# Performance work log

Hardware: AMD Instinct MI355X
Metric: run time of the kernel (lower is better)

Reference implementation:

```python
import jax, jax.numpy as jnp
import numpy as np

N = 50000          # total atoms in batch
E = 1_600_000      # total edges (flattened neighbor list)
ELEM = 64          # elem_fea_len
NBR = 32           # nbr_fea_len
EPS = 1e-5         # BatchNorm eps


def _batchnorm(x, gamma, beta):
    # training-mode BatchNorm1d: per-feature batch stats (biased variance)
    mean = x.mean(axis=0)
    var = ((x - mean) ** 2).mean(axis=0)
    return gamma * (x - mean) * jax.lax.rsqrt(var + EPS) + beta


def setup_inputs() -> dict:
    key = jax.random.key(0)
    ks = jax.random.split(key, 6)
    atom_in_fea = jax.random.normal(ks[0], (N, ELEM), jnp.float32)
    nbr_fea = jax.random.normal(ks[1], (E, NBR), jnp.float32)
    self_fea_idx = jnp.sort(jax.random.randint(ks[2], (E,), 0, N))
    nbr_fea_idx = jax.random.randint(ks[3], (E,), 0, N)
    fan_in = 2 * ELEM + NBR
    W = jax.random.normal(ks[4], (fan_in, 2 * ELEM), jnp.float32) * (1.0 / np.sqrt(fan_in))
    b = jnp.zeros((2 * ELEM,), jnp.float32)
    gamma1 = jnp.ones((2 * ELEM,), jnp.float32)
    beta1 = jnp.zeros((2 * ELEM,), jnp.float32)
    gamma2 = jnp.ones((ELEM,), jnp.float32)
    beta2 = jnp.zeros((ELEM,), jnp.float32)
    return {
        "atom_in_fea": atom_in_fea,
        "nbr_fea": nbr_fea,
        "self_fea_idx": self_fea_idx,
        "nbr_fea_idx": nbr_fea_idx,
        "W": W,
        "b": b,
        "gamma1": gamma1,
        "beta1": beta1,
        "gamma2": gamma2,
        "beta2": beta2,
    }


def reference(atom_in_fea, nbr_fea, self_fea_idx, nbr_fea_idx,
              W, b, gamma1, beta1, gamma2, beta2):
    # gather + concat: (E, 2*ELEM + NBR)
    total_fea = jnp.concatenate(
        [atom_in_fea[self_fea_idx], atom_in_fea[nbr_fea_idx], nbr_fea], axis=1)
    total_fea = total_fea @ W + b                    # fc_full: (E, 2*ELEM)
    total_fea = _batchnorm(total_fea, gamma1, beta1)  # bn1
    filter_fea, core_fea = jnp.split(total_fea, 2, axis=1)
    nbr_msg = jax.nn.sigmoid(filter_fea) * jax.nn.softplus(core_fea)  # (E, ELEM)
    nbr_sumed = jax.ops.segment_sum(nbr_msg, self_fea_idx, num_segments=N)
    nbr_sumed = _batchnorm(nbr_sumed, gamma2, beta2)  # bn2
    return jax.nn.softplus(atom_in_fea + nbr_sumed)   # residual + softplus2
```

## Files before the change

### kernel.cpp

```cpp
#include <hip/hip_runtime.h>

#define E_TOT 1600000
#define N_AT  50000
#define NB1   (E_TOT / 128)

typedef unsigned short u16;
typedef __attribute__((ext_vector_type(8))) __bf16 bf16x8;
typedef __attribute__((ext_vector_type(4))) __bf16 bf16x4;
typedef __attribute__((ext_vector_type(4))) float f32x4;

#define SUM1_OFF 0
#define SUM2_OFF 1024
#define WF_OFF   2048
#define NS_OFF   43008
#define AB_OFF   12843008
#define NBRB_OFF 19243008
#define PART_OFF 121643008

__device__ __forceinline__ u16 f2bf(float f) {
    unsigned int u = __float_as_uint(f);
    return (u16)((u + 0x7FFFu + ((u >> 16) & 1u)) >> 16);
}
__device__ __forceinline__ float softplus_f(float x) {
    return fmaxf(x, 0.0f) + __logf(1.0f + __expf(-fabsf(x)));
}
__device__ __forceinline__ bf16x8 cvt8v(f32x4 a, f32x4 b) {
    bf16x8 r;
    r[0] = (__bf16)a[0]; r[1] = (__bf16)a[1]; r[2] = (__bf16)a[2]; r[3] = (__bf16)a[3];
    r[4] = (__bf16)b[0]; r[5] = (__bf16)b[1]; r[6] = (__bf16)b[2]; r[7] = (__bf16)b[3];
    return r;
}
__device__ __forceinline__ void ldsdma16(void* lds, const void* g) {
    __builtin_amdgcn_global_load_lds(
        (const __attribute__((address_space(1))) unsigned int*)g,
        (__attribute__((address_space(3))) unsigned int*)lds, 16, 0, 0);
}

__global__ __launch_bounds__(256) void k_setup(const float* __restrict__ atom,
                                               const float* __restrict__ W,
                                               char* __restrict__ ws) {
    u16* wf   = (u16*)(ws + WF_OFF);
    float* ns = (float*)(ws + NS_OFF);
    u16* ab   = (u16*)(ws + AB_OFF);
    const int tid = blockIdx.x * 256 + threadIdx.x;
    const int gsz = gridDim.x * 256;

    for (int i = tid; i < 512; i += gsz) ((float*)ws)[i] = 0.0f;

    f32x4 z = {0.f, 0.f, 0.f, 0.f};
    for (int i = tid; i < N_AT * 64 / 4; i += gsz) ((f32x4*)ns)[i] = z;

    for (int i = tid; i < N_AT * 64 / 4; i += gsz) {
        f32x4 v = ((const f32x4*)atom)[i];
        bf16x4 h;
        h[0] = (__bf16)v[0]; h[1] = (__bf16)v[1];
        h[2] = (__bf16)v[2]; h[3] = (__bf16)v[3];
        *(bf16x4*)(ab + i * 4) = h;
    }

    for (int t = tid; t < 20480; t += gsz) {
        int j = t & 7, l2 = (t >> 3) & 63, ct = (t >> 9) & 7, kt = t >> 12;
        int k = kt * 32 + (l2 >> 4) * 8 + j;
        int c = ct * 16 + (l2 & 15);
        wf[t] = f2bf(W[k * 128 + c]);
    }
}

__global__ __launch_bounds__(512, 6) void k1_stats(const u16* __restrict__ ab,
                                                   const float* __restrict__ nbr,
                                                   u16* __restrict__ nbrb,
                                                   const int* __restrict__ sidx,
                                                   const int* __restrict__ nidx,
                                                   const u16* __restrict__ wf,
                                                   float* __restrict__ part) {
    __shared__ __align__(16) u16 bsm[20480];
    __shared__ float bs[256];
    const int tx = threadIdx.x, lane = tx & 63, w = tx >> 6;
    const int mrow = lane & 15, quad = lane >> 4;

#pragma unroll
    for (int i = 0; i < 5; i++) {
        int off = (i * 512 + tx) * 16;
        ldsdma16((char*)bsm + off, (const char*)wf + off);
    }

    const int r0 = blockIdx.x * 128 + w * 16 + mrow;
    const int s0 = sidx[r0];
    const int n0 = nidx[r0];
    const u16* pa0 = ab + (size_t)s0 * 64 + quad * 8;
    const u16* pb0 = ab + (size_t)n0 * 64 + quad * 8;
    const float* p0 = nbr + (size_t)r0 * 32 + quad * 8;

    bf16x8 a0 = *(const bf16x8*)(pa0);
    bf16x8 a1 = *(const bf16x8*)(pa0 + 32);
    bf16x8 a2 = *(const bf16x8*)(pb0);
    bf16x8 a3 = *(const bf16x8*)(pb0 + 32);
    bf16x8 a4 = cvt8v(*(const f32x4*)p0, *(const f32x4*)(p0 + 4));
    *(bf16x8*)(nbrb + (size_t)r0 * 32 + quad * 8) = a4;

    if (tx < 256) bs[tx] = 0.0f;
    __syncthreads();

    f32x4 acc[8];
#pragma unroll
    for (int ct = 0; ct < 8; ct++) { f32x4 z = {0.f, 0.f, 0.f, 0.f}; acc[ct] = z; }

#pragma unroll
    for (int kt = 0; kt < 5; kt++) {
        bf16x8 a = (kt == 0) ? a0 : (kt == 1) ? a1 : (kt == 2) ? a2 : (kt == 3) ? a3 : a4;
#pragma unroll
        for (int ct = 0; ct < 8; ct++) {
            bf16x8 b = *(const bf16x8*)&bsm[((kt * 8 + ct) * 64 + lane) * 8];
            acc[ct] = __builtin_amdgcn_mfma_f32_16x16x32_bf16(a, b, acc[ct], 0, 0, 0);
        }
    }

#pragma unroll
    for (int ct = 0; ct < 8; ct++) {
        float s = 0.f, q = 0.f;
#pragma unroll
        for (int rg = 0; rg < 4; rg++) {
            float v = acc[ct][rg];
            s += v; q += v * v;
        }
        s += __shfl_xor(s, 16, 64); s += __shfl_xor(s, 32, 64);
        q += __shfl_xor(q, 16, 64); q += __shfl_xor(q, 32, 64);
        if (quad == 0) {
            atomicAdd(&bs[ct * 16 + mrow], s);
            atomicAdd(&bs[128 + ct * 16 + mrow], q);
        }
    }
    __syncthreads();
    if (tx < 256) part[(size_t)blockIdx.x * 256 + tx] = bs[tx];
}

__global__ __launch_bounds__(256) void k2_red(const float* __restrict__ part,
                                              float* __restrict__ sums1) {
    const int tx = threadIdx.x;
    float s = 0.f;
    for (int r = blockIdx.x; r < NB1; r += 256) s += part[(size_t)r * 256 + tx];
    atomicAdd(&sums1[tx], s);
}

__global__ __launch_bounds__(512, 6) void k3_msg(const u16* __restrict__ ab,
                                                 const u16* __restrict__ nbrb,
                                                 const int* __restrict__ sidx,
                                                 const int* __restrict__ nidx,
                                                 const u16* __restrict__ wf,
                                                 const float* __restrict__ sums1,
                                                 const float* __restrict__ g1,
                                                 const float* __restrict__ b1,
                                                 float* __restrict__ ns) {
    __shared__ __align__(16) char smraw[40960];
    u16* bsm = (u16*)smraw;
    float (*msgb)[16 * 66] = (float(*)[16 * 66])smraw;
    const int tx = threadIdx.x, lane = tx & 63, w = tx >> 6;
    const int mrow = lane & 15, quad = lane >> 4;

#pragma unroll
    for (int i = 0; i < 5; i++) {
        int off = (i * 512 + tx) * 16;
        ldsdma16(smraw + off, (const char*)wf + off);
    }

    const int rb = blockIdx.x * 128 + w * 16;
    const int r0 = rb + mrow;
    const int s0 = sidx[r0];
    const int n0 = nidx[r0];
    const u16* pa0 = ab + (size_t)s0 * 64 + quad * 8;
    const u16* pb0 = ab + (size_t)n0 * 64 + quad * 8;

    bf16x8 a0 = *(const bf16x8*)(pa0);
    bf16x8 a1 = *(const bf16x8*)(pa0 + 32);
    bf16x8 a2 = *(const bf16x8*)(pb0);
    bf16x8 a3 = *(const bf16x8*)(pb0 + 32);
    bf16x8 a4 = *(const bf16x8*)(nbrb + (size_t)r0 * 32 + quad * 8);

    __syncthreads();

    f32x4 acc[8];
#pragma unroll
    for (int ct = 0; ct < 8; ct++) { f32x4 z = {0.f, 0.f, 0.f, 0.f}; acc[ct] = z; }

#pragma unroll
    for (int kt = 0; kt < 5; kt++) {
        bf16x8 a = (kt == 0) ? a0 : (kt == 1) ? a1 : (kt == 2) ? a2 : (kt == 3) ? a3 : a4;
#pragma unroll
        for (int ct = 0; ct < 8; ct++) {
            bf16x8 b = *(const bf16x8*)&bsm[((kt * 8 + ct) * 64 + lane) * 8];
            acc[ct] = __builtin_amdgcn_mfma_f32_16x16x32_bf16(a, b, acc[ct], 0, 0, 0);
        }
    }

    const float invE = 1.0f / (float)E_TOT;
    float af[4], kf[4], ac[4], kc[4];
#pragma unroll
    for (int ct = 0; ct < 4; ct++) {
        int cf = ct * 16 + mrow, cc = cf + 64;
        float mf = sums1[cf] * invE;
        float vf = sums1[128 + cf] * invE - mf * mf;
        af[ct] = g1[cf] * rsqrtf(vf + 1e-5f);
        kf[ct] = b1[cf] - af[ct] * mf;
        float mc = sums1[cc] * invE;
        float vc = sums1[128 + cc] * invE - mc * mc;
        ac[ct] = g1[cc] * rsqrtf(vc + 1e-5f);
        kc[ct] = b1[cc] - ac[ct] * mc;
    }

    __syncthreads();

    float* mw = msgb[w];
#pragma unroll
    for (int ct = 0; ct < 4; ct++) {
#pragma unroll
        for (int rg = 0; rg < 4; rg++) {
            float xf = af[ct] * acc[ct][rg] + kf[ct];
            float xc = ac[ct] * acc[ct + 4][rg] + kc[ct];
            float sg = 1.0f / (1.0f + __expf(-xf));
            mw[(quad * 4 + rg) * 66 + ct * 16 + mrow] = sg * softplus_f(xc);
        }
    }

    float accum = 0.f;
    int cur = sidx[rb];
#pragma unroll
    for (int i = 0; i < 16; i++) {
        int idx = sidx[rb + i];
        if (idx != cur) {
            atomicAdd(&ns[(size_t)cur * 64 + lane], accum);
            accum = 0.f;
            cur = idx;
        }
        accum += mw[i * 66 + lane];
    }
    atomicAdd(&ns[(size_t)cur * 64 + lane], accum);
}

__global__ __launch_bounds__(256) void k4_bn2stats(const float* __restrict__ ns,
                                                   float* __restrict__ sums2) {
    const int tx = threadIdx.x;
    const int col = tx & 63, rg = tx >> 6;
    float s = 0.f, q = 0.f;
    for (int r = blockIdx.x * 4 + rg; r < N_AT; r += 256 * 4) {
        float v = ns[r * 64 + col];
        s += v; q += v * v;
    }
    atomicAdd(&sums2[col], s);
    atomicAdd(&sums2[64 + col], q);
}

__global__ __launch_bounds__(256) void k5_final(const float* __restrict__ atom,
                                                const float* __restrict__ ns,
                                                const float* __restrict__ sums2,
                                                const float* __restrict__ g2,
                                                const float* __restrict__ b2,
                                                float* __restrict__ out) {
    const int i = blockIdx.x * 256 + threadIdx.x;
    const int col = i & 63;
    const float invN = 1.0f / (float)N_AT;
    float mean = sums2[col] * invN;
    float var = sums2[64 + col] * invN - mean * mean;
    float a2 = g2[col] * rsqrtf(var + 1e-5f);
    float c2 = b2[col] - a2 * mean;
    out[i] = softplus_f(atom[i] + a2 * ns[i] + c2);
}

extern "C" void kernel_launch(void* const* d_in, const int* in_sizes, int n_in,
                              void* d_out, int out_size, void* d_ws, size_t ws_size,
                              hipStream_t stream) {
    const float* atom = (const float*)d_in[0];
    const float* nbr  = (const float*)d_in[1];
    const int* sidx   = (const int*)d_in[2];
    const int* nidx   = (const int*)d_in[3];
    const float* W    = (const float*)d_in[4];
    const float* g1   = (const float*)d_in[6];
    const float* b1   = (const float*)d_in[7];
    const float* g2   = (const float*)d_in[8];
    const float* b2   = (const float*)d_in[9];
    float* out = (float*)d_out;

    char* ws = (char*)d_ws;
    float* sums1 = (float*)(ws + SUM1_OFF);
    float* sums2 = (float*)(ws + SUM2_OFF);
    u16*   wf    = (u16*)(ws + WF_OFF);
    float* nsum  = (float*)(ws + NS_OFF);
    u16*   ab    = (u16*)(ws + AB_OFF);
    u16*   nbrb  = (u16*)(ws + NBRB_OFF);
    float* part  = (float*)(ws + PART_OFF);

    k_setup<<<1024, 256, 0, stream>>>(atom, W, ws);
    k1_stats<<<NB1, 512, 0, stream>>>(ab, nbr, nbrb, sidx, nidx, wf, part);
    k2_red<<<256, 256, 0, stream>>>(part, sums1);
    k3_msg<<<NB1, 512, 0, stream>>>(ab, nbrb, sidx, nidx, wf, sums1, g1, b1, nsum);
    k4_bn2stats<<<256, 256, 0, stream>>>(nsum, sums2);
    k5_final<<<(N_AT * 64) / 256, 256, 0, stream>>>(atom, nsum, sums2, g2, b2, out);
}
```

Baseline: 709.2 us.

## Precompute per-atom projections of W and gather them per edge

```diff
diff --git a/kernel.cpp b/kernel.cpp
--- a/kernel.cpp
+++ b/kernel.cpp
@@ -6,20 +6,23 @@
 
 typedef unsigned short u16;
 typedef __attribute__((ext_vector_type(8))) __bf16 bf16x8;
-typedef __attribute__((ext_vector_type(4))) __bf16 bf16x4;
 typedef __attribute__((ext_vector_type(4))) float f32x4;
 
 #define SUM1_OFF 0
 #define SUM2_OFF 1024
-#define WF_OFF   2048
+#define WF3_OFF  2048
+#define WF12_OFF 10240
 #define NS_OFF   43008
-#define AB_OFF   12843008
-#define NBRB_OFF 19243008
-#define PART_OFF 121643008
+#define P12_OFF  12843008
+#define NBRB_OFF 38443008
+#define PART_OFF 140843008
 
 __device__ __forceinline__ u16 f2bf(float f) {
     unsigned int u = __float_as_uint(f);
     return (u16)((u + 0x7FFFu + ((u >> 16) & 1u)) >> 16);
+}
+__device__ __forceinline__ float bfu(u16 v) {
+    return __uint_as_float(((unsigned int)v) << 16);
 }
 __device__ __forceinline__ float softplus_f(float x) {
     return fmaxf(x, 0.0f) + __logf(1.0f + __expf(-fabsf(x)));
@@ -36,12 +39,11 @@
         (__attribute__((address_space(3))) unsigned int*)lds, 16, 0, 0);
 }
 
-__global__ __launch_bounds__(256) void k_setup(const float* __restrict__ atom,
-                                               const float* __restrict__ W,
+__global__ __launch_bounds__(256) void k_setup(const float* __restrict__ W,
                                                char* __restrict__ ws) {
-    u16* wf   = (u16*)(ws + WF_OFF);
+    u16* wf3  = (u16*)(ws + WF3_OFF);
+    u16* wf12 = (u16*)(ws + WF12_OFF);
     float* ns = (float*)(ws + NS_OFF);
-    u16* ab   = (u16*)(ws + AB_OFF);
     const int tid = blockIdx.x * 256 + threadIdx.x;
     const int gsz = gridDim.x * 256;
 
@@ -50,69 +52,113 @@
     f32x4 z = {0.f, 0.f, 0.f, 0.f};
     for (int i = tid; i < N_AT * 64 / 4; i += gsz) ((f32x4*)ns)[i] = z;
 
-    for (int i = tid; i < N_AT * 64 / 4; i += gsz) {
-        f32x4 v = ((const f32x4*)atom)[i];
-        bf16x4 h;
-        h[0] = (__bf16)v[0]; h[1] = (__bf16)v[1];
-        h[2] = (__bf16)v[2]; h[3] = (__bf16)v[3];
-        *(bf16x4*)(ab + i * 4) = h;
-    }
-
-    for (int t = tid; t < 20480; t += gsz) {
-        int j = t & 7, l2 = (t >> 3) & 63, ct = (t >> 9) & 7, kt = t >> 12;
+    for (int t = tid; t < 4096; t += gsz) {
+        int j = t & 7, l2 = (t >> 3) & 63, ct = (t >> 9) & 7;
+        int k = 128 + (l2 >> 4) * 8 + j;
+        int c = ct * 16 + (l2 & 15);
+        wf3[t] = f2bf(W[k * 128 + c]);
+    }
+    for (int t = tid; t < 16384; t += gsz) {
+        int j = t & 7, l2 = (t >> 3) & 63, ct = (t >> 9) & 15, kt = t >> 13;
         int k = kt * 32 + (l2 >> 4) * 8 + j;
         int c = ct * 16 + (l2 & 15);
-        wf[t] = f2bf(W[k * 128 + c]);
-    }
-}
-
-__global__ __launch_bounds__(512, 6) void k1_stats(const u16* __restrict__ ab,
-                                                   const float* __restrict__ nbr,
+        wf12[t] = f2bf(c < 128 ? W[k * 128 + c] : W[(64 + k) * 128 + (c - 128)]);
+    }
+}
+
+__global__ __launch_bounds__(512, 4) void k_p12(const float* __restrict__ atom,
+                                                const u16* __restrict__ wf12,
+                                                u16* __restrict__ p12) {
+    __shared__ __align__(16) u16 bsm[16384];
+    const int tx = threadIdx.x, lane = tx & 63, w = tx >> 6;
+    const int mrow = lane & 15, quad = lane >> 4;
+
+#pragma unroll
+    for (int i = 0; i < 4; i++) {
+        int off = (i * 512 + tx) * 16;
+        ldsdma16((char*)bsm + off, (const char*)wf12 + off);
+    }
+
+    const int rb = blockIdx.x * 128 + w * 16;
+    const int r0 = rb + mrow;
+    const int rr = r0 < N_AT ? r0 : N_AT - 1;
+    const float* pa = atom + (size_t)rr * 64 + quad * 8;
+
+    __syncthreads();
+
+    bf16x8 a0 = cvt8v(*(const f32x4*)pa, *(const f32x4*)(pa + 4));
+    bf16x8 a1 = cvt8v(*(const f32x4*)(pa + 32), *(const f32x4*)(pa + 36));
+
+    f32x4 acc[16];
+#pragma unroll
+    for (int ct = 0; ct < 16; ct++) { f32x4 zz = {0.f, 0.f, 0.f, 0.f}; acc[ct] = zz; }
+
+#pragma unroll
+    for (int kt = 0; kt < 2; kt++) {
+        bf16x8 a = kt ? a1 : a0;
+#pragma unroll
+        for (int ct = 0; ct < 16; ct++) {
+            bf16x8 b = *(const bf16x8*)&bsm[((kt * 16 + ct) * 64 + lane) * 8];
+            acc[ct] = __builtin_amdgcn_mfma_f32_16x16x32_bf16(a, b, acc[ct], 0, 0, 0);
+        }
+    }
+
+#pragma unroll
+    for (int ct = 0; ct < 16; ct++) {
+#pragma unroll
+        for (int rg = 0; rg < 4; rg++) {
+            int r = rb + quad * 4 + rg;
+            if (r < N_AT) p12[(size_t)r * 256 + ct * 16 + mrow] = f2bf(acc[ct][rg]);
+        }
+    }
+}
+
+__global__ __launch_bounds__(512, 6) void k1_stats(const float* __restrict__ nbr,
                                                    u16* __restrict__ nbrb,
                                                    const int* __restrict__ sidx,
                                                    const int* __restrict__ nidx,
-                                                   const u16* __restrict__ wf,
+                                                   const u16* __restrict__ wf3,
+                                                   const u16* __restrict__ p12,
                                                    float* __restrict__ part) {
-    __shared__ __align__(16) u16 bsm[20480];
+    __shared__ __align__(16) u16 bsm[4096];
     __shared__ float bs[256];
     const int tx = threadIdx.x, lane = tx & 63, w = tx >> 6;
     const int mrow = lane & 15, quad = lane >> 4;
 
-#pragma unroll
-    for (int i = 0; i < 5; i++) {
-        int off = (i * 512 + tx) * 16;
-        ldsdma16((char*)bsm + off, (const char*)wf + off);
-    }
-
-    const int r0 = blockIdx.x * 128 + w * 16 + mrow;
-    const int s0 = sidx[r0];
-    const int n0 = nidx[r0];
-    const u16* pa0 = ab + (size_t)s0 * 64 + quad * 8;
-    const u16* pb0 = ab + (size_t)n0 * 64 + quad * 8;
+    { int off = tx * 16; ldsdma16((char*)bsm + off, (const char*)wf3 + off); }
+
+    const int rb = blockIdx.x * 128 + w * 16;
+    const int r0 = rb + mrow;
+    const int e0 = rb + quad * 4;
+    int s_[4], n_[4];
+#pragma unroll
+    for (int rg = 0; rg < 4; rg++) { s_[rg] = sidx[e0 + rg]; n_[rg] = nidx[e0 + rg]; }
     const float* p0 = nbr + (size_t)r0 * 32 + quad * 8;
-
-    bf16x8 a0 = *(const bf16x8*)(pa0);
-    bf16x8 a1 = *(const bf16x8*)(pa0 + 32);
-    bf16x8 a2 = *(const bf16x8*)(pb0);
-    bf16x8 a3 = *(const bf16x8*)(pb0 + 32);
-    bf16x8 a4 = cvt8v(*(const f32x4*)p0, *(const f32x4*)(p0 + 4));
-    *(bf16x8*)(nbrb + (size_t)r0 * 32 + quad * 8) = a4;
 
     if (tx < 256) bs[tx] = 0.0f;
     __syncthreads();
 
+    f32x4 nlo = *(const f32x4*)p0;
+    f32x4 nhi = *(const f32x4*)(p0 + 4);
+    bf16x8 a4 = cvt8v(nlo, nhi);
+    *(bf16x8*)(nbrb + (size_t)r0 * 32 + quad * 8) = a4;
+
     f32x4 acc[8];
 #pragma unroll
-    for (int ct = 0; ct < 8; ct++) { f32x4 z = {0.f, 0.f, 0.f, 0.f}; acc[ct] = z; }
-
-#pragma unroll
-    for (int kt = 0; kt < 5; kt++) {
-        bf16x8 a = (kt == 0) ? a0 : (kt == 1) ? a1 : (kt == 2) ? a2 : (kt == 3) ? a3 : a4;
-#pragma unroll
-        for (int ct = 0; ct < 8; ct++) {
-            bf16x8 b = *(const bf16x8*)&bsm[((kt * 8 + ct) * 64 + lane) * 8];
-            acc[ct] = __builtin_amdgcn_mfma_f32_16x16x32_bf16(a, b, acc[ct], 0, 0, 0);
-        }
+    for (int ct = 0; ct < 8; ct++) { f32x4 zz = {0.f, 0.f, 0.f, 0.f}; acc[ct] = zz; }
+#pragma unroll
+    for (int ct = 0; ct < 8; ct++) {
+        bf16x8 b = *(const bf16x8*)&bsm[(ct * 64 + lane) * 8];
+        acc[ct] = __builtin_amdgcn_mfma_f32_16x16x32_bf16(a4, b, acc[ct], 0, 0, 0);
+    }
+
+#pragma unroll
+    for (int rg = 0; rg < 4; rg++) {
+        const u16* q1 = p12 + (size_t)s_[rg] * 256 + mrow;
+        const u16* q2 = p12 + (size_t)n_[rg] * 256 + 128 + mrow;
+#pragma unroll
+        for (int ct = 0; ct < 8; ct++)
+            acc[ct][rg] += bfu(q1[ct * 16]) + bfu(q2[ct * 16]);
     }
 
 #pragma unroll
@@ -142,54 +188,49 @@
     atomicAdd(&sums1[tx], s);
 }
 
-__global__ __launch_bounds__(512, 6) void k3_msg(const u16* __restrict__ ab,
-                                                 const u16* __restrict__ nbrb,
+__global__ __launch_bounds__(512, 6) void k3_msg(const u16* __restrict__ nbrb,
                                                  const int* __restrict__ sidx,
                                                  const int* __restrict__ nidx,
-                                                 const u16* __restrict__ wf,
+                                                 const u16* __restrict__ wf3,
+                                                 const u16* __restrict__ p12,
                                                  const float* __restrict__ sums1,
                                                  const float* __restrict__ g1,
                                                  const float* __restrict__ b1,
                                                  float* __restrict__ ns) {
-    __shared__ __align__(16) char smraw[40960];
-    u16* bsm = (u16*)smraw;
-    float (*msgb)[16 * 66] = (float(*)[16 * 66])smraw;
+    __shared__ __align__(16) u16 bsm[4096];
+    __shared__ float msgb[8][16 * 66];
     const int tx = threadIdx.x, lane = tx & 63, w = tx >> 6;
     const int mrow = lane & 15, quad = lane >> 4;
 
-#pragma unroll
-    for (int i = 0; i < 5; i++) {
-        int off = (i * 512 + tx) * 16;
-        ldsdma16(smraw + off, (const char*)wf + off);
-    }
+    { int off = tx * 16; ldsdma16((char*)bsm + off, (const char*)wf3 + off); }
 
     const int rb = blockIdx.x * 128 + w * 16;
     const int r0 = rb + mrow;
-    const int s0 = sidx[r0];
-    const int n0 = nidx[r0];
-    const u16* pa0 = ab + (size_t)s0 * 64 + quad * 8;
-    const u16* pb0 = ab + (size_t)n0 * 64 + quad * 8;
-
-    bf16x8 a0 = *(const bf16x8*)(pa0);
-    bf16x8 a1 = *(const bf16x8*)(pa0 + 32);
-    bf16x8 a2 = *(const bf16x8*)(pb0);
-    bf16x8 a3 = *(const bf16x8*)(pb0 + 32);
+    const int e0 = rb + quad * 4;
+    int s_[4], n_[4];
+#pragma unroll
+    for (int rg = 0; rg < 4; rg++) { s_[rg] = sidx[e0 + rg]; n_[rg] = nidx[e0 + rg]; }
+
+    __syncthreads();
+
     bf16x8 a4 = *(const bf16x8*)(nbrb + (size_t)r0 * 32 + quad * 8);
 
-    __syncthreads();
-
     f32x4 acc[8];
 #pragma unroll
-    for (int ct = 0; ct < 8; ct++) { f32x4 z = {0.f, 0.f, 0.f, 0.f}; acc[ct] = z; }
-
-#pragma unroll
-    for (int kt = 0; kt < 5; kt++) {
-        bf16x8 a = (kt == 0) ? a0 : (kt == 1) ? a1 : (kt == 2) ? a2 : (kt == 3) ? a3 : a4;
-#pragma unroll
-        for (int ct = 0; ct < 8; ct++) {
-            bf16x8 b = *(const bf16x8*)&bsm[((kt * 8 + ct) * 64 + lane) * 8];
-            acc[ct] = __builtin_amdgcn_mfma_f32_16x16x32_bf16(a, b, acc[ct], 0, 0, 0);
-        }
+    for (int ct = 0; ct < 8; ct++) { f32x4 zz = {0.f, 0.f, 0.f, 0.f}; acc[ct] = zz; }
+#pragma unroll
+    for (int ct = 0; ct < 8; ct++) {
+        bf16x8 b = *(const bf16x8*)&bsm[(ct * 64 + lane) * 8];
+        acc[ct] = __builtin_amdgcn_mfma_f32_16x16x32_bf16(a4, b, acc[ct], 0, 0, 0);
+    }
+
+#pragma unroll
+    for (int rg = 0; rg < 4; rg++) {
+        const u16* q1 = p12 + (size_t)s_[rg] * 256 + mrow;
+        const u16* q2 = p12 + (size_t)n_[rg] * 256 + 128 + mrow;
+#pragma unroll
+        for (int ct = 0; ct < 8; ct++)
+            acc[ct][rg] += bfu(q1[ct * 16]) + bfu(q2[ct * 16]);
     }
 
     const float invE = 1.0f / (float)E_TOT;
@@ -206,8 +247,6 @@
         ac[ct] = g1[cc] * rsqrtf(vc + 1e-5f);
         kc[ct] = b1[cc] - ac[ct] * mc;
     }
-
-    __syncthreads();
 
     float* mw = msgb[w];
 #pragma unroll
@@ -282,16 +321,18 @@
     char* ws = (char*)d_ws;
     float* sums1 = (float*)(ws + SUM1_OFF);
     float* sums2 = (float*)(ws + SUM2_OFF);
-    u16*   wf    = (u16*)(ws + WF_OFF);
+    u16*   wf3   = (u16*)(ws + WF3_OFF);
+    u16*   wf12  = (u16*)(ws + WF12_OFF);
     float* nsum  = (float*)(ws + NS_OFF);
-    u16*   ab    = (u16*)(ws + AB_OFF);
+    u16*   p12   = (u16*)(ws + P12_OFF);
     u16*   nbrb  = (u16*)(ws + NBRB_OFF);
     float* part  = (float*)(ws + PART_OFF);
 
-    k_setup<<<1024, 256, 0, stream>>>(atom, W, ws);
-    k1_stats<<<NB1, 512, 0, stream>>>(ab, nbr, nbrb, sidx, nidx, wf, part);
+    k_setup<<<512, 256, 0, stream>>>(W, ws);
+    k_p12<<<(N_AT + 127) / 128, 512, 0, stream>>>(atom, wf12, p12);
+    k1_stats<<<NB1, 512, 0, stream>>>(nbr, nbrb, sidx, nidx, wf3, p12, part);
     k2_red<<<256, 256, 0, stream>>>(part, sums1);
-    k3_msg<<<NB1, 512, 0, stream>>>(ab, nbrb, sidx, nidx, wf, sums1, g1, b1, nsum);
+    k3_msg<<<NB1, 512, 0, stream>>>(nbrb, sidx, nidx, wf3, p12, sums1, g1, b1, nsum);
     k4_bn2stats<<<256, 256, 0, stream>>>(nsum, sums2);
     k5_final<<<(N_AT * 64) / 256, 256, 0, stream>>>(atom, nsum, sums2, g2, b2, out);
 }
```

Result: slower. 934.1 us (+31.7%).

## Make edge-tile kernels persistent to amortize weight LDS loads and partials

Applied to the files above, without the earlier changes.

```diff
diff --git a/kernel.cpp b/kernel.cpp
--- a/kernel.cpp
+++ b/kernel.cpp
@@ -2,7 +2,9 @@
 
 #define E_TOT 1600000
 #define N_AT  50000
-#define NB1   (E_TOT / 128)
+#define NTILE (E_TOT / 128)
+#define NBP1  768
+#define NBP3  512
 
 typedef unsigned short u16;
 typedef __attribute__((ext_vector_type(8))) __bf16 bf16x8;
@@ -83,46 +85,58 @@
         int off = (i * 512 + tx) * 16;
         ldsdma16((char*)bsm + off, (const char*)wf + off);
     }
-
-    const int r0 = blockIdx.x * 128 + w * 16 + mrow;
-    const int s0 = sidx[r0];
-    const int n0 = nidx[r0];
-    const u16* pa0 = ab + (size_t)s0 * 64 + quad * 8;
-    const u16* pb0 = ab + (size_t)n0 * 64 + quad * 8;
-    const float* p0 = nbr + (size_t)r0 * 32 + quad * 8;
-
-    bf16x8 a0 = *(const bf16x8*)(pa0);
-    bf16x8 a1 = *(const bf16x8*)(pa0 + 32);
-    bf16x8 a2 = *(const bf16x8*)(pb0);
-    bf16x8 a3 = *(const bf16x8*)(pb0 + 32);
-    bf16x8 a4 = cvt8v(*(const f32x4*)p0, *(const f32x4*)(p0 + 4));
-    *(bf16x8*)(nbrb + (size_t)r0 * 32 + quad * 8) = a4;
-
     if (tx < 256) bs[tx] = 0.0f;
+
+    const int rl = w * 16 + mrow;
+    float sa[8], qa[8];
+#pragma unroll
+    for (int ct = 0; ct < 8; ct++) { sa[ct] = 0.f; qa[ct] = 0.f; }
+
+    int sNxt = sidx[blockIdx.x * 128 + rl];
+    int nNxt = nidx[blockIdx.x * 128 + rl];
     __syncthreads();
 
-    f32x4 acc[8];
-#pragma unroll
-    for (int ct = 0; ct < 8; ct++) { f32x4 z = {0.f, 0.f, 0.f, 0.f}; acc[ct] = z; }
-
-#pragma unroll
-    for (int kt = 0; kt < 5; kt++) {
-        bf16x8 a = (kt == 0) ? a0 : (kt == 1) ? a1 : (kt == 2) ? a2 : (kt == 3) ? a3 : a4;
+    for (int t = blockIdx.x; t < NTILE; t += NBP1) {
+        const int r0 = t * 128 + rl;
+        const int s0 = sNxt, n0 = nNxt;
+        const int tn = t + NBP1;
+        if (tn < NTILE) { sNxt = sidx[tn * 128 + rl]; nNxt = nidx[tn * 128 + rl]; }
+
+        const u16* pa0 = ab + (size_t)s0 * 64 + quad * 8;
+        const u16* pb0 = ab + (size_t)n0 * 64 + quad * 8;
+        const float* p0 = nbr + (size_t)r0 * 32 + quad * 8;
+        bf16x8 a2 = *(const bf16x8*)(pb0);
+        bf16x8 a3 = *(const bf16x8*)(pb0 + 32);
+        bf16x8 a0 = *(const bf16x8*)(pa0);
+        bf16x8 a1 = *(const bf16x8*)(pa0 + 32);
+        bf16x8 a4 = cvt8v(*(const f32x4*)p0, *(const f32x4*)(p0 + 4));
+        *(bf16x8*)(nbrb + (size_t)r0 * 32 + quad * 8) = a4;
+
+        f32x4 acc[8];
+#pragma unroll
+        for (int ct = 0; ct < 8; ct++) { f32x4 zz = {0.f, 0.f, 0.f, 0.f}; acc[ct] = zz; }
+#pragma unroll
+        for (int kt = 0; kt < 5; kt++) {
+            bf16x8 a = (kt == 0) ? a0 : (kt == 1) ? a1 : (kt == 2) ? a2 : (kt == 3) ? a3 : a4;
+#pragma unroll
+            for (int ct = 0; ct < 8; ct++) {
+                bf16x8 b = *(const bf16x8*)&bsm[((kt * 8 + ct) * 64 + lane) * 8];
+                acc[ct] = __builtin_amdgcn_mfma_f32_16x16x32_bf16(a, b, acc[ct], 0, 0, 0);
+            }
+        }
 #pragma unroll
         for (int ct = 0; ct < 8; ct++) {
-            bf16x8 b = *(const bf16x8*)&bsm[((kt * 8 + ct) * 64 + lane) * 8];
-            acc[ct] = __builtin_amdgcn_mfma_f32_16x16x32_bf16(a, b, acc[ct], 0, 0, 0);
+#pragma unroll
+            for (int rg = 0; rg < 4; rg++) {
+                float v = acc[ct][rg];
+                sa[ct] += v; qa[ct] += v * v;
+            }
         }
     }
 
 #pragma unroll
     for (int ct = 0; ct < 8; ct++) {
-        float s = 0.f, q = 0.f;
-#pragma unroll
-        for (int rg = 0; rg < 4; rg++) {
-            float v = acc[ct][rg];
-            s += v; q += v * v;
-        }
+        float s = sa[ct], q = qa[ct];
         s += __shfl_xor(s, 16, 64); s += __shfl_xor(s, 32, 64);
         q += __shfl_xor(q, 16, 64); q += __shfl_xor(q, 32, 64);
         if (quad == 0) {
@@ -138,11 +152,11 @@
                                               float* __restrict__ sums1) {
     const int tx = threadIdx.x;
     float s = 0.f;
-    for (int r = blockIdx.x; r < NB1; r += 256) s += part[(size_t)r * 256 + tx];
+    for (int r = blockIdx.x; r < NBP1; r += 256) s += part[(size_t)r * 256 + tx];
     atomicAdd(&sums1[tx], s);
 }
 
-__global__ __launch_bounds__(512, 6) void k3_msg(const u16* __restrict__ ab,
+__global__ __launch_bounds__(512, 4) void k3_msg(const u16* __restrict__ ab,
                                                  const u16* __restrict__ nbrb,
                                                  const int* __restrict__ sidx,
                                                  const int* __restrict__ nidx,
@@ -151,45 +165,15 @@
                                                  const float* __restrict__ g1,
                                                  const float* __restrict__ b1,
                                                  float* __restrict__ ns) {
-    __shared__ __align__(16) char smraw[40960];
-    u16* bsm = (u16*)smraw;
-    float (*msgb)[16 * 66] = (float(*)[16 * 66])smraw;
+    __shared__ __align__(16) u16 bsm[20480];
+    __shared__ float msgb[8][16 * 66];
     const int tx = threadIdx.x, lane = tx & 63, w = tx >> 6;
     const int mrow = lane & 15, quad = lane >> 4;
 
 #pragma unroll
     for (int i = 0; i < 5; i++) {
         int off = (i * 512 + tx) * 16;
-        ldsdma16(smraw + off, (const char*)wf + off);
-    }
-
-    const int rb = blockIdx.x * 128 + w * 16;
-    const int r0 = rb + mrow;
-    const int s0 = sidx[r0];
-    const int n0 = nidx[r0];
-    const u16* pa0 = ab + (size_t)s0 * 64 + quad * 8;
-    const u16* pb0 = ab + (size_t)n0 * 64 + quad * 8;
-
-    bf16x8 a0 = *(const bf16x8*)(pa0);
-    bf16x8 a1 = *(const bf16x8*)(pa0 + 32);
-    bf16x8 a2 = *(const bf16x8*)(pb0);
-    bf16x8 a3 = *(const bf16x8*)(pb0 + 32);
-    bf16x8 a4 = *(const bf16x8*)(nbrb + (size_t)r0 * 32 + quad * 8);
-
-    __syncthreads();
-
-    f32x4 acc[8];
-#pragma unroll
-    for (int ct = 0; ct < 8; ct++) { f32x4 z = {0.f, 0.f, 0.f, 0.f}; acc[ct] = z; }
-
-#pragma unroll
-    for (int kt = 0; kt < 5; kt++) {
-        bf16x8 a = (kt == 0) ? a0 : (kt == 1) ? a1 : (kt == 2) ? a2 : (kt == 3) ? a3 : a4;
-#pragma unroll
-        for (int ct = 0; ct < 8; ct++) {
-            bf16x8 b = *(const bf16x8*)&bsm[((kt * 8 + ct) * 64 + lane) * 8];
-            acc[ct] = __builtin_amdgcn_mfma_f32_16x16x32_bf16(a, b, acc[ct], 0, 0, 0);
-        }
+        ldsdma16((char*)bsm + off, (const char*)wf + off);
     }
 
     const float invE = 1.0f / (float)E_TOT;
@@ -207,33 +191,65 @@
         kc[ct] = b1[cc] - ac[ct] * mc;
     }
 
+    const int rl = w * 16 + mrow;
+    int sNxt = sidx[blockIdx.x * 128 + rl];
+    int nNxt = nidx[blockIdx.x * 128 + rl];
     __syncthreads();
 
     float* mw = msgb[w];
-#pragma unroll
-    for (int ct = 0; ct < 4; ct++) {
-#pragma unroll
-        for (int rg = 0; rg < 4; rg++) {
-            float xf = af[ct] * acc[ct][rg] + kf[ct];
-            float xc = ac[ct] * acc[ct + 4][rg] + kc[ct];
-            float sg = 1.0f / (1.0f + __expf(-xf));
-            mw[(quad * 4 + rg) * 66 + ct * 16 + mrow] = sg * softplus_f(xc);
-        }
-    }
-
-    float accum = 0.f;
-    int cur = sidx[rb];
-#pragma unroll
-    for (int i = 0; i < 16; i++) {
-        int idx = sidx[rb + i];
-        if (idx != cur) {
-            atomicAdd(&ns[(size_t)cur * 64 + lane], accum);
-            accum = 0.f;
-            cur = idx;
-        }
-        accum += mw[i * 66 + lane];
-    }
-    atomicAdd(&ns[(size_t)cur * 64 + lane], accum);
+    for (int t = blockIdx.x; t < NTILE; t += NBP3) {
+        const int rb = t * 128 + w * 16;
+        const int r0 = rb + mrow;
+        const int s0 = sNxt, n0 = nNxt;
+        const int tn = t + NBP3;
+        if (tn < NTILE) { sNxt = sidx[tn * 128 + rl]; nNxt = nidx[tn * 128 + rl]; }
+
+        const u16* pa0 = ab + (size_t)s0 * 64 + quad * 8;
+        const u16* pb0 = ab + (size_t)n0 * 64 + quad * 8;
+        bf16x8 a2 = *(const bf16x8*)(pb0);
+        bf16x8 a3 = *(const bf16x8*)(pb0 + 32);
+        bf16x8 a0 = *(const bf16x8*)(pa0);
+        bf16x8 a1 = *(const bf16x8*)(pa0 + 32);
+        bf16x8 a4 = *(const bf16x8*)(nbrb + (size_t)r0 * 32 + quad * 8);
+
+        f32x4 acc[8];
+#pragma unroll
+        for (int ct = 0; ct < 8; ct++) { f32x4 zz = {0.f, 0.f, 0.f, 0.f}; acc[ct] = zz; }
+#pragma unroll
+        for (int kt = 0; kt < 5; kt++) {
+            bf16x8 a = (kt == 0) ? a0 : (kt == 1) ? a1 : (kt == 2) ? a2 : (kt == 3) ? a3 : a4;
+#pragma unroll
+            for (int ct = 0; ct < 8; ct++) {
+                bf16x8 b = *(const bf16x8*)&bsm[((kt * 8 + ct) * 64 + lane) * 8];
+                acc[ct] = __builtin_amdgcn_mfma_f32_16x16x32_bf16(a, b, acc[ct], 0, 0, 0);
+            }
+        }
+
+#pragma unroll
+        for (int ct = 0; ct < 4; ct++) {
+#pragma unroll
+            for (int rg = 0; rg < 4; rg++) {
+                float xf = af[ct] * acc[ct][rg] + kf[ct];
+                float xc = ac[ct] * acc[ct + 4][rg] + kc[ct];
+                float sg = 1.0f / (1.0f + __expf(-xf));
+                mw[(quad * 4 + rg) * 66 + ct * 16 + mrow] = sg * softplus_f(xc);
+            }
+        }
+
+        float accum = 0.f;
+        int cur = sidx[rb];
+#pragma unroll
+        for (int i = 0; i < 16; i++) {
+            int idx = sidx[rb + i];
+            if (idx != cur) {
+                atomicAdd(&ns[(size_t)cur * 64 + lane], accum);
+                accum = 0.f;
+                cur = idx;
+            }
+            accum += mw[i * 66 + lane];
+        }
+        atomicAdd(&ns[(size_t)cur * 64 + lane], accum);
+    }
 }
 
 __global__ __launch_bounds__(256) void k4_bn2stats(const float* __restrict__ ns,
@@ -289,9 +305,9 @@
     float* part  = (float*)(ws + PART_OFF);
 
     k_setup<<<1024, 256, 0, stream>>>(atom, W, ws);
-    k1_stats<<<NB1, 512, 0, stream>>>(ab, nbr, nbrb, sidx, nidx, wf, part);
+    k1_stats<<<NBP1, 512, 0, stream>>>(ab, nbr, nbrb, sidx, nidx, wf, part);
     k2_red<<<256, 256, 0, stream>>>(part, sums1);
-    k3_msg<<<NB1, 512, 0, stream>>>(ab, nbrb, sidx, nidx, wf, sums1, g1, b1, nsum);
+    k3_msg<<<NBP3, 512, 0, stream>>>(ab, nbrb, sidx, nidx, wf, sums1, g1, b1, nsum);
     k4_bn2stats<<<256, 256, 0, stream>>>(nsum, sums2);
     k5_final<<<(N_AT * 64) / 256, 256, 0, stream>>>(atom, nsum, sums2, g2, b2, out);
 }
```

Measured after the change: 1.584 ms. 123% more time.
